# Kernel optimization log

Measured on AMD Instinct MI355X. Metric: run time of the kernel, lower is better.

The kernel has to match this reference:

```python
import jax, jax.numpy as jnp
import numpy as np

IN_FEATURES = 4096
OUT_FEATURES = 12288


def setup_inputs() -> dict:
    key = jax.random.key(0)
    k1, k2, k3 = jax.random.split(key, 3)
    inp = jax.random.normal(k1, (2, 2048, IN_FEATURES), dtype=jnp.float32)
    # int8 quantized weight, [out_features, in_features]
    quant_w = jax.random.randint(k2, (OUT_FEATURES, IN_FEATURES), -128, 128, dtype=jnp.int32).astype(jnp.int8)
    # per-output-channel scale, small positive (typical ~ max|w|/127)
    scale_w = (jax.random.uniform(k3, (OUT_FEATURES,), dtype=jnp.float32) + 0.5) * 0.02
    return {"inp": inp, "quant_w": quant_w, "scale_w": scale_w}


def reference(inp, quant_w, scale_w):
    # extract_weight_to_half: dequantize int8 weight with per-channel scale
    weight = quant_w.astype(inp.dtype) * scale_w[:, None]        # [N, K]
    # inp.view(-1, K) @ weight.T, reshaped back -> fuse via einsum
    out = jnp.einsum("bsk,nk->bsn", inp, weight)                 # [B, S, N]
    return out
```

## Files before the change

### kernel.cpp

```cpp
#include <hip/hip_runtime.h>
#include <hip/hip_bf16.h>


#define K_DIM 4096
#define N_DIM 12288

constexpr int BM = 256;
constexpr int BN = 128;
constexpr int BKB = 64;
constexpr int NT = K_DIM / BKB;

typedef float  f32x4  __attribute__((ext_vector_type(4)));
typedef int    i32x4  __attribute__((ext_vector_type(4)));
typedef short  bf16x8 __attribute__((ext_vector_type(8)));
typedef unsigned short u16x4 __attribute__((ext_vector_type(4)));

__device__ __forceinline__ unsigned short f32_to_bf16(float f) {
    unsigned int u = __builtin_bit_cast(unsigned int, f);
    u += 0x7FFFu + ((u >> 16) & 1u);
    return (unsigned short)(u >> 16);
}


__global__ __launch_bounds__(256)
void quant_a_kernel(const float* __restrict__ A,
                    signed char* __restrict__ Aq,
                    float* __restrict__ Ra) {
    const int row  = blockIdx.x;
    const int tid  = threadIdx.x;
    const int lane = tid & 63;
    const int wid  = tid >> 6;
    const float* arow = A + (size_t)row * K_DIM;
    const int base = tid * 16;

    f32x4 v[4];
    #pragma unroll
    for (int i = 0; i < 4; ++i)
        v[i] = *(const f32x4*)(arow + base + i * 4);

    float mx = 0.f;
    #pragma unroll
    for (int i = 0; i < 4; ++i)
        #pragma unroll
        for (int j = 0; j < 4; ++j)
            mx = fmaxf(mx, fabsf(v[i][j]));

    #pragma unroll
    for (int off = 32; off > 0; off >>= 1)
        mx = fmaxf(mx, __shfl_xor(mx, off));

    __shared__ float wmax[4];
    if (lane == 0) wmax[wid] = mx;
    __syncthreads();
    mx = fmaxf(fmaxf(wmax[0], wmax[1]), fmaxf(wmax[2], wmax[3]));

    const float inv = (mx > 0.f) ? (127.0f / mx) : 0.f;
    if (tid == 0) Ra[row] = mx * (1.0f / 127.0f);

    int p[4];
    #pragma unroll
    for (int i = 0; i < 4; ++i) {
        int b0 = (int)rintf(v[i][0] * inv);
        int b1 = (int)rintf(v[i][1] * inv);
        int b2 = (int)rintf(v[i][2] * inv);
        int b3 = (int)rintf(v[i][3] * inv);
        p[i] = (b0 & 255) | ((b1 & 255) << 8) | ((b2 & 255) << 16) | (b3 << 24);
    }
    *(i32x4*)(Aq + (size_t)row * K_DIM + base) = *(i32x4*)p;
}


__global__ __launch_bounds__(256)
void cvt_w8_kernel(const int* __restrict__ W, signed char* __restrict__ Wq, int n16) {
    int stride = gridDim.x * blockDim.x;
    for (int i = blockIdx.x * blockDim.x + threadIdx.x; i < n16; i += stride) {
        const int* src = W + (size_t)i * 16;
        int p[4];
        #pragma unroll
        for (int q = 0; q < 4; ++q) {
            const i32x4 w = *(const i32x4*)(src + q * 4);
            p[q] = (w[0] & 255) | ((w[1] & 255) << 8) | ((w[2] & 255) << 16) | (w[3] << 24);
        }
        *(i32x4*)(Wq + (size_t)i * 16) = *(i32x4*)p;
    }
}


__device__ __forceinline__ void gload_lds16(const void* g, void* l) {
    __builtin_amdgcn_global_load_lds(
        (const __attribute__((address_space(1))) unsigned int*)g,
        (__attribute__((address_space(3))) unsigned int*)l,
        16, 0, 0);
}

__global__ __launch_bounds__(256, 2)
void gemm_i8_2b(const signed char* __restrict__ Aq,
                const signed char* __restrict__ Wq,
                const float* __restrict__ Sw,
                const float* __restrict__ Ra,
                float* __restrict__ Out,
                int M) {
    __shared__ __align__(16) unsigned char As8[2][BM * BKB];
    __shared__ __align__(16) unsigned char Bs8[2][BN * BKB];

    const int tid  = threadIdx.x;
    const int lane = tid & 63;
    const int wid  = tid >> 6;
    const int wm   = wid >> 1;
    const int wn   = wid & 1;

    const int nwgy = M / BM;
    const int nwg  = (N_DIM / BN) * nwgy;
    const int cpx  = nwg >> 3;
    const int bid  = blockIdx.x;
    const int swz  = (bid & 7) * cpx + (bid >> 3);
    const int bx   = swz / nwgy;
    const int by   = swz % nwgy;
    const int bm   = by * BM;
    const int bn   = bx * BN;

    const int sr   = lane & 15;
    const int sc16 = (((lane >> 4) ^ (lane & 3)) * 16);

    #define STG_A(k0B, L)                                                            \
        _Pragma("unroll") for (int i_ = 0; i_ < 4; ++i_)                            \
            gload_lds16(Aq + (size_t)(bm + (i_ * 4 + wid) * 16 + sr) * K_DIM        \
                            + (k0B) + sc16,                                         \
                        (L) + (i_ * 4 + wid) * 1024);
    #define STG_B(k0B, L)                                                            \
        _Pragma("unroll") for (int i_ = 0; i_ < 2; ++i_)                            \
            gload_lds16(Wq + (size_t)(bn + (i_ * 4 + wid) * 16 + sr) * K_DIM        \
                            + (k0B) + sc16,                                         \
                        (L) + (i_ * 4 + wid) * 1024);

    i32x4 acc[8][4];
    #pragma unroll
    for (int i = 0; i < 8; ++i)
        #pragma unroll
        for (int j = 0; j < 4; ++j)
            acc[i][j] = (i32x4){0, 0, 0, 0};

    const int fro = ((((lane >> 4) ^ (lane & 3)) << 8) | ((lane & 15) << 4));

    STG_A(0, &As8[0][0]);
    STG_B(0, &Bs8[0][0]);
    __syncthreads();

    for (int t = 0; t < NT; ++t) {
        const int cur = t & 1;

        i32x4 af[8];
        i32x4 bf[4];
        #pragma unroll
        for (int mf = 0; mf < 8; ++mf)
            af[mf] = *(const i32x4*)&As8[cur][(wm * 8 + mf) * 1024 + fro];
        #pragma unroll
        for (int nf = 0; nf < 4; ++nf)
            bf[nf] = *(const i32x4*)&Bs8[cur][(wn * 4 + nf) * 1024 + fro];

        if (t + 1 < NT) {
            const int k1 = (t + 1) * BKB;
            STG_A(k1, &As8[cur ^ 1][0]);
            STG_B(k1, &Bs8[cur ^ 1][0]);
        }

        __builtin_amdgcn_s_setprio(1);
        #pragma unroll
        for (int mf = 0; mf < 8; ++mf)
            #pragma unroll
            for (int nf = 0; nf < 4; ++nf)
                acc[mf][nf] = __builtin_amdgcn_mfma_i32_16x16x64_i8(
                    af[mf], bf[nf], acc[mf][nf], 0, 0, 0);
        __builtin_amdgcn_s_setprio(0);

        __syncthreads();
    }
    #undef STG_A
    #undef STG_B

    const int c0 = lane & 15;
    const int r0 = (lane >> 4) * 4;
    float rav[8][4];
    #pragma unroll
    for (int mf = 0; mf < 8; ++mf)
        #pragma unroll
        for (int j = 0; j < 4; ++j)
            rav[mf][j] = Ra[bm + wm * 128 + mf * 16 + r0 + j];

    #pragma unroll
    for (int nf = 0; nf < 4; ++nf) {
        const int col = bn + wn * 64 + nf * 16 + c0;
        const float s = Sw[col];
        #pragma unroll
        for (int mf = 0; mf < 8; ++mf) {
            const int rowb = bm + wm * 128 + mf * 16 + r0;
            #pragma unroll
            for (int j = 0; j < 4; ++j)
                Out[(size_t)(rowb + j) * N_DIM + col] = (float)acc[mf][nf][j] * s * rav[mf][j];
        }
    }
}


constexpr int FBM = 128, FBN = 128, FBK = 64, FPAD = 8;

__global__ __launch_bounds__(256)
void qlinear_fused_kernel(const float* __restrict__ A, const int* __restrict__ Wqi,
                          const float* __restrict__ Sw, float* __restrict__ Out, int M) {
    __shared__ unsigned short Asf[FBM][FBK + FPAD];
    __shared__ unsigned short Bsf[FBN][FBK + FPAD];
    const int tid  = threadIdx.x;
    const int lane = tid & 63;
    const int wid  = tid >> 6;
    const int wm   = wid >> 1;
    const int wn   = wid & 1;
    const int bm = blockIdx.y * FBM;
    const int bn = blockIdx.x * FBN;
    const int rowT = tid >> 4;
    const int kq   = tid & 15;
    f32x4 acc[4][4];
    #pragma unroll
    for (int i = 0; i < 4; ++i)
        #pragma unroll
        for (int j = 0; j < 4; ++j) acc[i][j] = (f32x4){0.f,0.f,0.f,0.f};
    const int c0 = lane & 15;
    const int kg = (lane >> 4) * 8;
    for (int k0 = 0; k0 < K_DIM; k0 += FBK) {
        #pragma unroll
        for (int it = 0; it < 8; ++it) {
            const int r = it * 16 + rowT;
            const f32x4 a4 = *(const f32x4*)(A + (size_t)(bm + r) * K_DIM + k0 + kq * 4);
            u16x4 h;
            h[0]=f32_to_bf16(a4[0]); h[1]=f32_to_bf16(a4[1]);
            h[2]=f32_to_bf16(a4[2]); h[3]=f32_to_bf16(a4[3]);
            *(u16x4*)&Asf[r][kq*4] = h;
        }
        #pragma unroll
        for (int it = 0; it < 8; ++it) {
            const int r = it * 16 + rowT;
            const i32x4 w4 = *(const i32x4*)(Wqi + (size_t)(bn + r) * K_DIM + k0 + kq * 4);
            u16x4 h;
            h[0]=f32_to_bf16((float)w4[0]); h[1]=f32_to_bf16((float)w4[1]);
            h[2]=f32_to_bf16((float)w4[2]); h[3]=f32_to_bf16((float)w4[3]);
            *(u16x4*)&Bsf[r][kq*4] = h;
        }
        __syncthreads();
        #pragma unroll
        for (int ks = 0; ks < 2; ++ks) {
            const int kk = ks * 32 + kg;
            bf16x8 af2[4], bfr[4];
            #pragma unroll
            for (int mf = 0; mf < 4; ++mf)
                af2[mf] = *(const bf16x8*)&Asf[wm*64 + mf*16 + c0][kk];
            #pragma unroll
            for (int nf = 0; nf < 4; ++nf)
                bfr[nf] = *(const bf16x8*)&Bsf[wn*64 + nf*16 + c0][kk];
            #pragma unroll
            for (int mf = 0; mf < 4; ++mf)
                #pragma unroll
                for (int nf = 0; nf < 4; ++nf)
                    acc[mf][nf] = __builtin_amdgcn_mfma_f32_16x16x32_bf16(
                        af2[mf], bfr[nf], acc[mf][nf], 0, 0, 0);
        }
        __syncthreads();
    }
    const int r0 = (lane >> 4) * 4;
    #pragma unroll
    for (int nf = 0; nf < 4; ++nf) {
        const int col = bn + wn*64 + nf*16 + c0;
        const float s = Sw[col];
        #pragma unroll
        for (int mf = 0; mf < 4; ++mf) {
            const int rowb = bm + wm*64 + mf*16 + r0;
            #pragma unroll
            for (int j = 0; j < 4; ++j)
                Out[(size_t)(rowb + j) * N_DIM + col] = acc[mf][nf][j] * s;
        }
    }
}

extern "C" void kernel_launch(void* const* d_in, const int* in_sizes, int n_in,
                              void* d_out, int out_size, void* d_ws, size_t ws_size,
                              hipStream_t stream) {
    const float* inp = (const float*)d_in[0];
    const int*   qw  = (const int*)d_in[1];
    const float* sw  = (const float*)d_in[2];
    float*       out = (float*)d_out;

    const int M = in_sizes[0] / K_DIM;
    const size_t nA = (size_t)M * K_DIM;
    const size_t nW = (size_t)N_DIM * K_DIM;
    const size_t needQ = nA + nW + (size_t)M * sizeof(float);

    if (ws_size >= needQ && (M % BM) == 0) {
        signed char* Aq  = (signed char*)d_ws;
        signed char* Wq8 = Aq + nA;
        float*       Ra  = (float*)(Wq8 + nW);
        quant_a_kernel<<<M, 256, 0, stream>>>(inp, Aq, Ra);
        cvt_w8_kernel<<<2048, 256, 0, stream>>>(qw, Wq8, (int)(nW / 16));
        dim3 grid((N_DIM / BN) * (M / BM));
        gemm_i8_2b<<<grid, 256, 0, stream>>>(Aq, Wq8, sw, Ra, out, M);
    } else {
        dim3 grid(N_DIM / FBN, M / FBM);
        qlinear_fused_kernel<<<grid, 256, 0, stream>>>(inp, qw, sw, out, M);
    }
}
```

Measured before the change: 313.2 us.

## Switch int8 GEMM to 32x32x32 MFMA tiles with remapped LDS fragment loads

Replaces the 16x16x64 int8 MFMA with the 32x32x32 variant: each wave now holds 4x2 accumulators of 16 ints and issues two k-steps per 64-byte K tile, with new swizzled LDS offsets and a matching epilogue layout. Larger MFMA tiles need fewer LDS fragment reads per FLOP and fewer instruction issues. The epilogue now reads the activation scale Ra directly per element rather than preloading it. The risk is a wrong fragment mapping or LDS bank conflicts from the new addressing.

```diff
diff --git a/kernel.cpp b/kernel.cpp
--- a/kernel.cpp
+++ b/kernel.cpp
@@ -10,9 +10,10 @@
 constexpr int BKB = 64;
 constexpr int NT = K_DIM / BKB;
 
-typedef float  f32x4  __attribute__((ext_vector_type(4)));
-typedef int    i32x4  __attribute__((ext_vector_type(4)));
-typedef short  bf16x8 __attribute__((ext_vector_type(8)));
+typedef float  f32x4   __attribute__((ext_vector_type(4)));
+typedef int    i32x4   __attribute__((ext_vector_type(4)));
+typedef int    i32x16  __attribute__((ext_vector_type(16)));
+typedef short  bf16x8  __attribute__((ext_vector_type(8)));
 typedef unsigned short u16x4 __attribute__((ext_vector_type(4)));
 
 __device__ __forceinline__ unsigned short f32_to_bf16(float f) {
@@ -94,12 +95,12 @@
 }
 
 __global__ __launch_bounds__(256, 2)
-void gemm_i8_2b(const signed char* __restrict__ Aq,
-                const signed char* __restrict__ Wq,
-                const float* __restrict__ Sw,
-                const float* __restrict__ Ra,
-                float* __restrict__ Out,
-                int M) {
+void gemm_i8_2b32(const signed char* __restrict__ Aq,
+                  const signed char* __restrict__ Wq,
+                  const float* __restrict__ Sw,
+                  const float* __restrict__ Ra,
+                  float* __restrict__ Out,
+                  int M) {
     __shared__ __align__(16) unsigned char As8[2][BM * BKB];
     __shared__ __align__(16) unsigned char Bs8[2][BN * BKB];
 
@@ -133,14 +134,23 @@
                             + (k0B) + sc16,                                         \
                         (L) + (i_ * 4 + wid) * 1024);
 
-    i32x4 acc[8][4];
-    #pragma unroll
-    for (int i = 0; i < 8; ++i)
-        #pragma unroll
-        for (int j = 0; j < 4; ++j)
-            acc[i][j] = (i32x4){0, 0, 0, 0};
-
-    const int fro = ((((lane >> 4) ^ (lane & 3)) << 8) | ((lane & 15) << 4));
+    i32x16 acc[4][2];
+    #pragma unroll
+    for (int i = 0; i < 4; ++i)
+        #pragma unroll
+        for (int j = 0; j < 2; ++j)
+            #pragma unroll
+            for (int e = 0; e < 16; ++e)
+                acc[i][j][e] = 0;
+
+    const int r4 = lane & 15;
+    const int ch = (lane >> 4) & 1;
+    const int kh = lane >> 5;
+
+    #define AOFF(mf, ks) ((wm * 8 + (mf) * 2 + ch) * 1024 + \
+        (((((ks) * 2 + kh) ^ (lane & 3)) << 4 | r4) << 4))
+    #define BOFF(nf, ks) ((wn * 4 + (nf) * 2 + ch) * 1024 + \
+        (((((ks) * 2 + kh) ^ (lane & 3)) << 4 | r4) << 4))
 
     STG_A(0, &As8[0][0]);
     STG_B(0, &Bs8[0][0]);
@@ -149,14 +159,18 @@
     for (int t = 0; t < NT; ++t) {
         const int cur = t & 1;
 
-        i32x4 af[8];
-        i32x4 bf[4];
-        #pragma unroll
-        for (int mf = 0; mf < 8; ++mf)
-            af[mf] = *(const i32x4*)&As8[cur][(wm * 8 + mf) * 1024 + fro];
-        #pragma unroll
-        for (int nf = 0; nf < 4; ++nf)
-            bf[nf] = *(const i32x4*)&Bs8[cur][(wn * 4 + nf) * 1024 + fro];
+        i32x4 af[4][2];
+        i32x4 bf[2][2];
+        #pragma unroll
+        for (int mf = 0; mf < 4; ++mf)
+            #pragma unroll
+            for (int ks = 0; ks < 2; ++ks)
+                af[mf][ks] = *(const i32x4*)&As8[cur][AOFF(mf, ks)];
+        #pragma unroll
+        for (int nf = 0; nf < 2; ++nf)
+            #pragma unroll
+            for (int ks = 0; ks < 2; ++ks)
+                bf[nf][ks] = *(const i32x4*)&Bs8[cur][BOFF(nf, ks)];
 
         if (t + 1 < NT) {
             const int k1 = (t + 1) * BKB;
@@ -166,37 +180,35 @@
 
         __builtin_amdgcn_s_setprio(1);
         #pragma unroll
-        for (int mf = 0; mf < 8; ++mf)
-            #pragma unroll
-            for (int nf = 0; nf < 4; ++nf)
-                acc[mf][nf] = __builtin_amdgcn_mfma_i32_16x16x64_i8(
-                    af[mf], bf[nf], acc[mf][nf], 0, 0, 0);
+        for (int ks = 0; ks < 2; ++ks)
+            #pragma unroll
+            for (int mf = 0; mf < 4; ++mf)
+                #pragma unroll
+                for (int nf = 0; nf < 2; ++nf)
+                    acc[mf][nf] = __builtin_amdgcn_mfma_i32_32x32x32_i8(
+                        af[mf][ks], bf[nf][ks], acc[mf][nf], 0, 0, 0);
         __builtin_amdgcn_s_setprio(0);
 
         __syncthreads();
     }
     #undef STG_A
     #undef STG_B
-
-    const int c0 = lane & 15;
-    const int r0 = (lane >> 4) * 4;
-    float rav[8][4];
-    #pragma unroll
-    for (int mf = 0; mf < 8; ++mf)
-        #pragma unroll
-        for (int j = 0; j < 4; ++j)
-            rav[mf][j] = Ra[bm + wm * 128 + mf * 16 + r0 + j];
-
-    #pragma unroll
-    for (int nf = 0; nf < 4; ++nf) {
-        const int col = bn + wn * 64 + nf * 16 + c0;
+    #undef AOFF
+    #undef BOFF
+
+    const int c0 = lane & 31;
+    #pragma unroll
+    for (int nf = 0; nf < 2; ++nf) {
+        const int col = bn + wn * 64 + nf * 32 + c0;
         const float s = Sw[col];
         #pragma unroll
-        for (int mf = 0; mf < 8; ++mf) {
-            const int rowb = bm + wm * 128 + mf * 16 + r0;
-            #pragma unroll
-            for (int j = 0; j < 4; ++j)
-                Out[(size_t)(rowb + j) * N_DIM + col] = (float)acc[mf][nf][j] * s * rav[mf][j];
+        for (int mf = 0; mf < 4; ++mf) {
+            const int rowb = bm + wm * 128 + mf * 32 + 4 * kh;
+            #pragma unroll
+            for (int reg = 0; reg < 16; ++reg) {
+                const int row = rowb + (reg & 3) + 8 * (reg >> 2);
+                Out[(size_t)row * N_DIM + col] = (float)acc[mf][nf][reg] * s * Ra[row];
+            }
         }
     }
 }
@@ -299,7 +311,7 @@
         quant_a_kernel<<<M, 256, 0, stream>>>(inp, Aq, Ra);
         cvt_w8_kernel<<<2048, 256, 0, stream>>>(qw, Wq8, (int)(nW / 16));
         dim3 grid((N_DIM / BN) * (M / BM));
-        gemm_i8_2b<<<grid, 256, 0, stream>>>(Aq, Wq8, sw, Ra, out, M);
+        gemm_i8_2b32<<<grid, 256, 0, stream>>>(Aq, Wq8, sw, Ra, out, M);
     } else {
         dim3 grid(N_DIM / FBN, M / FBM);
         qlinear_fused_kernel<<<grid, 256, 0, stream>>>(inp, qw, sw, out, M);
```

Measured after the change: 323.6 us. 1.03x slower.
